# Performance work log

Hardware: AMD Instinct MI355X
Metric: run time of the kernel (lower is better)

The kernel has to match this reference:

```python
import jax, jax.numpy as jnp
import numpy as np

V = 8192
E = 262144
IN_DIM = 128
OUT_DIM = 128
NEG_SLOPE = 0.2


def setup_inputs() -> dict:
    key = jax.random.key(0)
    k1, k2, k3, k4 = jax.random.split(key, 4)
    h = jax.random.normal(k1, (V, IN_DIM), dtype=jnp.float32)
    edge_index = jax.random.randint(k2, (2, E), 0, V, dtype=jnp.int64)
    # nn.Linear weights: W (out_dim, in_dim), att (1, 2*out_dim), both bias-free
    W = jax.random.normal(k3, (OUT_DIM, IN_DIM), dtype=jnp.float32) / np.sqrt(IN_DIM)
    att_w = jax.random.normal(k4, (1, 2 * OUT_DIM), dtype=jnp.float32) / np.sqrt(2 * OUT_DIM)
    return {"h": h, "edge_index": edge_index, "W": W, "att_w": att_w}


def reference(h, edge_index, W, att_w):
    # h: (V, in_dim) -> (V, out_dim)
    hw = h @ W.T
    src, dst = edge_index[0], edge_index[1]
    # edge features: concat of endpoint embeddings -> (E, 2*out_dim)
    e = jnp.concatenate([hw[src], hw[dst]], axis=-1)
    # attention logits per edge, LeakyReLU(0.2)
    a = jax.nn.leaky_relu(jnp.squeeze(e @ att_w.T, -1), negative_slope=NEG_SLOPE)
    v = hw.shape[0]
    # faithful to original: dense V x V matrix, zeros on non-edges,
    # softmax over ALL columns (non-edges included as score 0)
    alpha = jnp.zeros((v, v), dtype=hw.dtype).at[src, dst].set(a)
    alpha = jax.nn.softmax(alpha, axis=-1)
    # dropout is identity in eval mode (deterministic reference)
    return alpha @ hw
```

## Files before the change

kernel.cpp:

```cpp
#include <hip/hip_runtime.h>
#include <hip/hip_bf16.h>
#include <math.h>


#define V 8192
#define E 262144
#define D 128
#define NEG_SLOPE 0.2f
#define CAP 96

#define FMA4(acc, hv, wv) { acc.x += (hv)*(wv).x; acc.y += (hv)*(wv).y; \
                            acc.z += (hv)*(wv).z; acc.w += (hv)*(wv).w; }

__device__ __forceinline__ unsigned short f2bf(float f) {
    unsigned u = __float_as_uint(f);
    return (unsigned short)((u + 0x7fffu + ((u >> 16) & 1u)) >> 16);
}
__device__ __forceinline__ float bf2f_low(int p) {
    return __uint_as_float(((unsigned)p) << 16);
}

__global__ __launch_bounds__(256) void k_hw(const float* __restrict__ h,
                                            const float* __restrict__ W,
                                            const float* __restrict__ att,
                                            unsigned short* __restrict__ hwb,
                                            float* __restrict__ s1,
                                            float* __restrict__ s2,
                                            float* __restrict__ Pb,
                                            int* __restrict__ cnt) {
    __shared__ float Wt[D * 132];
    __shared__ float hs[16][D];
    __shared__ float atts[2 * D];
    int t = threadIdx.x, b = blockIdx.x;
    int g0 = b * 256 + t;
    if (g0 < V) cnt[g0] = 0;
    atts[t] = att[t];
    for (int f4 = t; f4 < (D * D) / 4; f4 += 256) {
        int o = f4 >> 5, k = (f4 * 4) & 127;
        float4 wv = *(const float4*)&W[o * D + k];
        Wt[(k + 0) * 132 + o] = wv.x;
        Wt[(k + 1) * 132 + o] = wv.y;
        Wt[(k + 2) * 132 + o] = wv.z;
        Wt[(k + 3) * 132 + o] = wv.w;
    }
    int r0 = b * 16;
    {
        int row = t >> 5, col = (t * 4) & 127;
        *(float4*)&hs[row][col]     = *(const float4*)&h[(r0 + row) * D + col];
        *(float4*)&hs[row + 8][col] = *(const float4*)&h[(r0 + row + 8) * D + col];
    }
    __syncthreads();

    int c4 = (t & 31) * 4;
    int rq = t >> 5;
    float4 acc0 = make_float4(0.f, 0.f, 0.f, 0.f);
    float4 acc1 = make_float4(0.f, 0.f, 0.f, 0.f);
    #pragma unroll 2
    for (int kq = 0; kq < D; kq += 4) {
        float4 ha = *(const float4*)&hs[rq][kq];
        float4 hb = *(const float4*)&hs[rq + 8][kq];
        float4 w0 = *(const float4*)&Wt[(kq + 0) * 132 + c4];
        float4 w1 = *(const float4*)&Wt[(kq + 1) * 132 + c4];
        float4 w2 = *(const float4*)&Wt[(kq + 2) * 132 + c4];
        float4 w3 = *(const float4*)&Wt[(kq + 3) * 132 + c4];
        FMA4(acc0, ha.x, w0); FMA4(acc0, ha.y, w1);
        FMA4(acc0, ha.z, w2); FMA4(acc0, ha.w, w3);
        FMA4(acc1, hb.x, w0); FMA4(acc1, hb.y, w1);
        FMA4(acc1, hb.z, w2); FMA4(acc1, hb.w, w3);
    }
    int rowa = r0 + rq, rowb = r0 + rq + 8;
    ushort4 pa = make_ushort4(f2bf(acc0.x), f2bf(acc0.y), f2bf(acc0.z), f2bf(acc0.w));
    ushort4 pb = make_ushort4(f2bf(acc1.x), f2bf(acc1.y), f2bf(acc1.z), f2bf(acc1.w));
    *(ushort4*)&hwb[rowa * D + c4] = pa;
    *(ushort4*)&hwb[rowb * D + c4] = pb;

    float p1a = acc0.x * atts[c4] + acc0.y * atts[c4 + 1] + acc0.z * atts[c4 + 2] + acc0.w * atts[c4 + 3];
    float p2a = acc0.x * atts[D + c4] + acc0.y * atts[D + c4 + 1] + acc0.z * atts[D + c4 + 2] + acc0.w * atts[D + c4 + 3];
    float p1b = acc1.x * atts[c4] + acc1.y * atts[c4 + 1] + acc1.z * atts[c4 + 2] + acc1.w * atts[c4 + 3];
    float p2b = acc1.x * atts[D + c4] + acc1.y * atts[D + c4 + 1] + acc1.z * atts[D + c4 + 2] + acc1.w * atts[D + c4 + 3];
    #pragma unroll
    for (int m = 16; m; m >>= 1) {
        p1a += __shfl_xor(p1a, m); p2a += __shfl_xor(p2a, m);
        p1b += __shfl_xor(p1b, m); p2b += __shfl_xor(p2b, m);
    }
    if ((t & 31) == 0) {
        s1[rowa] = p1a; s2[rowa] = p2a;
        s1[rowb] = p1b; s2[rowb] = p2b;
    }

    __syncthreads();
    float* scr = &hs[0][0];
    scr[rq * D + c4 + 0] = acc0.x + acc1.x;
    scr[rq * D + c4 + 1] = acc0.y + acc1.y;
    scr[rq * D + c4 + 2] = acc0.z + acc1.z;
    scr[rq * D + c4 + 3] = acc0.w + acc1.w;
    __syncthreads();
    if (t < D) {
        float s = 0.f;
        #pragma unroll
        for (int r = 0; r < 8; ++r) s += scr[r * D + t];
        Pb[b * D + t] = s;
    }
}

__global__ __launch_bounds__(256) void k_scatter(const int* __restrict__ ei,
                                                 const float* __restrict__ s1,
                                                 const float* __restrict__ s2,
                                                 int* __restrict__ cnt,
                                                 int* __restrict__ bucket,
                                                 const float* __restrict__ Pb,
                                                 float* __restrict__ S) {
    int b = blockIdx.x, t = threadIdx.x;
    if (b < 256) {
        int g = b * 256 + t;
        int4 sv = *(const int4*)&ei[4 * g];
        int4 dv = *(const int4*)&ei[E + 4 * g];
        const int* sp = &sv.x;
        const int* dp = &dv.x;
        #pragma unroll
        for (int j = 0; j < 4; ++j) {
            int src = sp[j], dst = dp[j];
            float a = s1[src] + s2[dst];
            a = a > 0.f ? a : NEG_SLOPE * a;
            float w = expf(a) - 1.f;
            int pos = atomicAdd(&cnt[src], 1);
            if (pos < CAP)
                bucket[src * CAP + pos] = (dst << 16) | (int)f2bf(w);
        }
    } else {
        __shared__ float red[256];
        int c = t & 127, half = t >> 7;
        float s = 0.f;
        #pragma unroll 4
        for (int r = half; r < 512; r += 2)
            s += Pb[r * D + c];
        red[t] = s;
        __syncthreads();
        if (t < D) S[t] = red[t] + red[D + t];
    }
}

__global__ __launch_bounds__(256) void k_row(const int* __restrict__ bucket,
                                             const int* __restrict__ cnt,
                                             const unsigned short* __restrict__ hwb,
                                             const float* __restrict__ S,
                                             float* __restrict__ out) {
    int t = threadIdx.x;
    int wv = t >> 6, lane = t & 63;
    int row = blockIdx.x * 4 + wv;
    int deg = cnt[row];
    if (deg > CAP) deg = CAP;
    const int* bk = bucket + row * CAP;
    int e0 = bk[lane];
    int e1 = (lane < CAP - 64) ? bk[64 + lane] : 0;
    int p0 = (lane < deg)      ? e0 : (int)0xFFFF0000;
    int p1 = (64 + lane < deg) ? e1 : (int)0xFFFF0000;
    int d0 = p0 >> 16;
    int d1 = p1 >> 16;
    int n0 = deg < 64 ? deg : 64;
    float2 acc = make_float2(0.f, 0.f);
    float dex = 0.f;
    for (int j = 0; j < n0; ++j) {
        int pj = __shfl(p0, j);
        int dj = pj >> 16;
        float wj = bf2f_low(pj);
        unsigned long long m = __ballot(d0 == dj);
        if (m & ((1ull << j) - 1ull)) wj = 0.f;
        unsigned hv = *(const unsigned*)&hwb[dj * D + lane * 2];
        acc.x += wj * __uint_as_float(hv << 16);
        acc.y += wj * __uint_as_float(hv & 0xFFFF0000u);
        dex += wj;
    }
    for (int j = 64; j < deg; ++j) {
        int pj = __shfl(p1, j - 64);
        int dj = pj >> 16;
        float wj = bf2f_low(pj);
        unsigned long long m0 = __ballot(d0 == dj);
        unsigned long long m1 = __ballot(d1 == dj) & ((1ull << (j - 64)) - 1ull);
        if (m0 | m1) wj = 0.f;
        unsigned hv = *(const unsigned*)&hwb[dj * D + lane * 2];
        acc.x += wj * __uint_as_float(hv << 16);
        acc.y += wj * __uint_as_float(hv & 0xFFFF0000u);
        dex += wj;
    }
    float inv = 1.f / ((float)V + dex);
    float2 s = *(const float2*)&S[lane * 2];
    float2 o;
    o.x = (s.x + acc.x) * inv;
    o.y = (s.y + acc.y) * inv;
    *(float2*)&out[row * D + lane * 2] = o;
}

extern "C" void kernel_launch(void* const* d_in, const int* in_sizes, int n_in,
                              void* d_out, int out_size, void* d_ws, size_t ws_size,
                              hipStream_t stream) {
    const float* h   = (const float*)d_in[0];
    const int*   ei  = (const int*)d_in[1];
    const float* W   = (const float*)d_in[2];
    const float* att = (const float*)d_in[3];
    float* out = (float*)d_out;

    char* ws = (char*)d_ws;
    unsigned short* hwb = (unsigned short*)(ws);
    float* s1  = (float*)(ws + 2097152);
    float* s2  = (float*)(ws + 2129920);
    float* S   = (float*)(ws + 2162688);
    int*   cnt = (int*)(ws + 2163200);
    int*   bucket = (int*)(ws + 2195968);
    float* Pb  = (float*)(ws + 5341696);

    k_hw     <<<512,  256, 0, stream>>>(h, W, att, hwb, s1, s2, Pb, cnt);
    k_scatter<<<257,  256, 0, stream>>>(ei, s1, s2, cnt, bucket, Pb, S);
    k_row    <<<2048, 256, 0, stream>>>(bucket, cnt, hwb, S, out);
}
```

Baseline: 118.2 us.

## Rebalance hw tiling, one-edge-per-thread scatter, unroll row gather via LDS

The projection kernel now computes 32 rows per block with half the blocks, reading h directly from global memory, which halves the redundant W transpose work per row. The scatter kernel processes one edge per thread across four times as many blocks to spread the atomics out. The row kernel stages each row's bucket in shared memory and unrolls the neighbour gather by four so several hw loads are in flight at once. The trade-off is higher register pressure and uncoalesced global reads of h in the GEMM.

Result: faster. 106.0 us (-10.3%).

```diff
diff --git a/kernel.cpp b/kernel.cpp
--- a/kernel.cpp
+++ b/kernel.cpp
@@ -29,71 +29,78 @@
                                             float* __restrict__ Pb,
                                             int* __restrict__ cnt) {
     __shared__ float Wt[D * 132];
-    __shared__ float hs[16][D];
     __shared__ float atts[2 * D];
+    __shared__ float scr[8 * D];
     int t = threadIdx.x, b = blockIdx.x;
-    int g0 = b * 256 + t;
-    if (g0 < V) cnt[g0] = 0;
+    if (b < 32) cnt[b * 256 + t] = 0;
     atts[t] = att[t];
     for (int f4 = t; f4 < (D * D) / 4; f4 += 256) {
-        int o = f4 >> 5, k = (f4 * 4) & 127;
+        int o = f4 >> 5, k = (f4 & 31) * 4;
         float4 wv = *(const float4*)&W[o * D + k];
         Wt[(k + 0) * 132 + o] = wv.x;
         Wt[(k + 1) * 132 + o] = wv.y;
         Wt[(k + 2) * 132 + o] = wv.z;
         Wt[(k + 3) * 132 + o] = wv.w;
     }
-    int r0 = b * 16;
-    {
-        int row = t >> 5, col = (t * 4) & 127;
-        *(float4*)&hs[row][col]     = *(const float4*)&h[(r0 + row) * D + col];
-        *(float4*)&hs[row + 8][col] = *(const float4*)&h[(r0 + row + 8) * D + col];
-    }
     __syncthreads();
 
     int c4 = (t & 31) * 4;
     int rq = t >> 5;
-    float4 acc0 = make_float4(0.f, 0.f, 0.f, 0.f);
-    float4 acc1 = make_float4(0.f, 0.f, 0.f, 0.f);
-    #pragma unroll 2
+    int r0 = b * 32;
+    float4 a0 = make_float4(0.f,0.f,0.f,0.f), a1 = a0, a2 = a0, a3 = a0;
+    const float* h0p = &h[(r0 + rq     ) * D];
+    const float* h1p = &h[(r0 + rq +  8) * D];
+    const float* h2p = &h[(r0 + rq + 16) * D];
+    const float* h3p = &h[(r0 + rq + 24) * D];
+    #pragma unroll 4
     for (int kq = 0; kq < D; kq += 4) {
-        float4 ha = *(const float4*)&hs[rq][kq];
-        float4 hb = *(const float4*)&hs[rq + 8][kq];
         float4 w0 = *(const float4*)&Wt[(kq + 0) * 132 + c4];
         float4 w1 = *(const float4*)&Wt[(kq + 1) * 132 + c4];
         float4 w2 = *(const float4*)&Wt[(kq + 2) * 132 + c4];
         float4 w3 = *(const float4*)&Wt[(kq + 3) * 132 + c4];
-        FMA4(acc0, ha.x, w0); FMA4(acc0, ha.y, w1);
-        FMA4(acc0, ha.z, w2); FMA4(acc0, ha.w, w3);
-        FMA4(acc1, hb.x, w0); FMA4(acc1, hb.y, w1);
-        FMA4(acc1, hb.z, w2); FMA4(acc1, hb.w, w3);
-    }
-    int rowa = r0 + rq, rowb = r0 + rq + 8;
-    ushort4 pa = make_ushort4(f2bf(acc0.x), f2bf(acc0.y), f2bf(acc0.z), f2bf(acc0.w));
-    ushort4 pb = make_ushort4(f2bf(acc1.x), f2bf(acc1.y), f2bf(acc1.z), f2bf(acc1.w));
-    *(ushort4*)&hwb[rowa * D + c4] = pa;
-    *(ushort4*)&hwb[rowb * D + c4] = pb;
-
-    float p1a = acc0.x * atts[c4] + acc0.y * atts[c4 + 1] + acc0.z * atts[c4 + 2] + acc0.w * atts[c4 + 3];
-    float p2a = acc0.x * atts[D + c4] + acc0.y * atts[D + c4 + 1] + acc0.z * atts[D + c4 + 2] + acc0.w * atts[D + c4 + 3];
-    float p1b = acc1.x * atts[c4] + acc1.y * atts[c4 + 1] + acc1.z * atts[c4 + 2] + acc1.w * atts[c4 + 3];
-    float p2b = acc1.x * atts[D + c4] + acc1.y * atts[D + c4 + 1] + acc1.z * atts[D + c4 + 2] + acc1.w * atts[D + c4 + 3];
+        float4 hv;
+        hv = *(const float4*)&h0p[kq];
+        FMA4(a0, hv.x, w0); FMA4(a0, hv.y, w1); FMA4(a0, hv.z, w2); FMA4(a0, hv.w, w3);
+        hv = *(const float4*)&h1p[kq];
+        FMA4(a1, hv.x, w0); FMA4(a1, hv.y, w1); FMA4(a1, hv.z, w2); FMA4(a1, hv.w, w3);
+        hv = *(const float4*)&h2p[kq];
+        FMA4(a2, hv.x, w0); FMA4(a2, hv.y, w1); FMA4(a2, hv.z, w2); FMA4(a2, hv.w, w3);
+        hv = *(const float4*)&h3p[kq];
+        FMA4(a3, hv.x, w0); FMA4(a3, hv.y, w1); FMA4(a3, hv.z, w2); FMA4(a3, hv.w, w3);
+    }
+    *(ushort4*)&hwb[(r0 + rq     ) * D + c4] = make_ushort4(f2bf(a0.x), f2bf(a0.y), f2bf(a0.z), f2bf(a0.w));
+    *(ushort4*)&hwb[(r0 + rq +  8) * D + c4] = make_ushort4(f2bf(a1.x), f2bf(a1.y), f2bf(a1.z), f2bf(a1.w));
+    *(ushort4*)&hwb[(r0 + rq + 16) * D + c4] = make_ushort4(f2bf(a2.x), f2bf(a2.y), f2bf(a2.z), f2bf(a2.w));
+    *(ushort4*)&hwb[(r0 + rq + 24) * D + c4] = make_ushort4(f2bf(a3.x), f2bf(a3.y), f2bf(a3.z), f2bf(a3.w));
+
+    float q1[4], q2[4];
+    float4* accs[4] = {&a0, &a1, &a2, &a3};
+    #pragma unroll
+    for (int r = 0; r < 4; ++r) {
+        float4 v = *accs[r];
+        q1[r] = v.x * atts[c4] + v.y * atts[c4 + 1] + v.z * atts[c4 + 2] + v.w * atts[c4 + 3];
+        q2[r] = v.x * atts[D + c4] + v.y * atts[D + c4 + 1] + v.z * atts[D + c4 + 2] + v.w * atts[D + c4 + 3];
+    }
     #pragma unroll
     for (int m = 16; m; m >>= 1) {
-        p1a += __shfl_xor(p1a, m); p2a += __shfl_xor(p2a, m);
-        p1b += __shfl_xor(p1b, m); p2b += __shfl_xor(p2b, m);
+        #pragma unroll
+        for (int r = 0; r < 4; ++r) {
+            q1[r] += __shfl_xor(q1[r], m);
+            q2[r] += __shfl_xor(q2[r], m);
+        }
     }
     if ((t & 31) == 0) {
-        s1[rowa] = p1a; s2[rowa] = p2a;
-        s1[rowb] = p1b; s2[rowb] = p2b;
-    }
-
-    __syncthreads();
-    float* scr = &hs[0][0];
-    scr[rq * D + c4 + 0] = acc0.x + acc1.x;
-    scr[rq * D + c4 + 1] = acc0.y + acc1.y;
-    scr[rq * D + c4 + 2] = acc0.z + acc1.z;
-    scr[rq * D + c4 + 3] = acc0.w + acc1.w;
+        #pragma unroll
+        for (int r = 0; r < 4; ++r) {
+            s1[r0 + rq + r * 8] = q1[r];
+            s2[r0 + rq + r * 8] = q2[r];
+        }
+    }
+
+    scr[rq * D + c4 + 0] = a0.x + a1.x + a2.x + a3.x;
+    scr[rq * D + c4 + 1] = a0.y + a1.y + a2.y + a3.y;
+    scr[rq * D + c4 + 2] = a0.z + a1.z + a2.z + a3.z;
+    scr[rq * D + c4 + 3] = a0.w + a1.w + a2.w + a3.w;
     __syncthreads();
     if (t < D) {
         float s = 0.f;
@@ -111,28 +118,22 @@
                                                  const float* __restrict__ Pb,
                                                  float* __restrict__ S) {
     int b = blockIdx.x, t = threadIdx.x;
-    if (b < 256) {
+    if (b < 1024) {
         int g = b * 256 + t;
-        int4 sv = *(const int4*)&ei[4 * g];
-        int4 dv = *(const int4*)&ei[E + 4 * g];
-        const int* sp = &sv.x;
-        const int* dp = &dv.x;
-        #pragma unroll
-        for (int j = 0; j < 4; ++j) {
-            int src = sp[j], dst = dp[j];
-            float a = s1[src] + s2[dst];
-            a = a > 0.f ? a : NEG_SLOPE * a;
-            float w = expf(a) - 1.f;
-            int pos = atomicAdd(&cnt[src], 1);
-            if (pos < CAP)
-                bucket[src * CAP + pos] = (dst << 16) | (int)f2bf(w);
-        }
+        int src = ei[g];
+        int dst = ei[E + g];
+        float a = s1[src] + s2[dst];
+        a = a > 0.f ? a : NEG_SLOPE * a;
+        float w = expf(a) - 1.f;
+        int pos = atomicAdd(&cnt[src], 1);
+        if (pos < CAP)
+            bucket[src * CAP + pos] = (dst << 16) | (int)f2bf(w);
     } else {
         __shared__ float red[256];
         int c = t & 127, half = t >> 7;
         float s = 0.f;
         #pragma unroll 4
-        for (int r = half; r < 512; r += 2)
+        for (int r = half; r < 256; r += 2)
             s += Pb[r * D + c];
         red[t] = s;
         __syncthreads();
@@ -145,6 +146,7 @@
                                              const unsigned short* __restrict__ hwb,
                                              const float* __restrict__ S,
                                              float* __restrict__ out) {
+    __shared__ int lb[4][CAP];
     int t = threadIdx.x;
     int wv = t >> 6, lane = t & 63;
     int row = blockIdx.x * 4 + wv;
@@ -155,40 +157,69 @@
     int e1 = (lane < CAP - 64) ? bk[64 + lane] : 0;
     int p0 = (lane < deg)      ? e0 : (int)0xFFFF0000;
     int p1 = (64 + lane < deg) ? e1 : (int)0xFFFF0000;
+    lb[wv][lane] = p0;
+    if (lane < CAP - 64) lb[wv][64 + lane] = p1;
     int d0 = p0 >> 16;
     int d1 = p1 >> 16;
     int n0 = deg < 64 ? deg : 64;
-    float2 acc = make_float2(0.f, 0.f);
-    float dex = 0.f;
-    for (int j = 0; j < n0; ++j) {
-        int pj = __shfl(p0, j);
+    float accx = 0.f, accy = 0.f, dex = 0.f;
+    const int* myb = lb[wv];
+    int col2 = lane * 2;
+    int j = 0;
+    for (; j + 4 <= n0; j += 4) {
+        int4 pq = *(const int4*)&myb[j];
+        int dj0 = pq.x >> 16, dj1 = pq.y >> 16, dj2 = pq.z >> 16, dj3 = pq.w >> 16;
+        unsigned hv0 = *(const unsigned*)&hwb[dj0 * D + col2];
+        unsigned hv1 = *(const unsigned*)&hwb[dj1 * D + col2];
+        unsigned hv2 = *(const unsigned*)&hwb[dj2 * D + col2];
+        unsigned hv3 = *(const unsigned*)&hwb[dj3 * D + col2];
+        unsigned long long m0 = __ballot(d0 == dj0);
+        unsigned long long m1 = __ballot(d0 == dj1);
+        unsigned long long m2 = __ballot(d0 == dj2);
+        unsigned long long m3 = __ballot(d0 == dj3);
+        float w0 = (m0 & ((1ull << (j + 0)) - 1ull)) ? 0.f : bf2f_low(pq.x);
+        float w1 = (m1 & ((1ull << (j + 1)) - 1ull)) ? 0.f : bf2f_low(pq.y);
+        float w2 = (m2 & ((1ull << (j + 2)) - 1ull)) ? 0.f : bf2f_low(pq.z);
+        float w3 = (m3 & ((1ull << (j + 3)) - 1ull)) ? 0.f : bf2f_low(pq.w);
+        accx += w0 * __uint_as_float(hv0 << 16);
+        accy += w0 * __uint_as_float(hv0 & 0xFFFF0000u);
+        accx += w1 * __uint_as_float(hv1 << 16);
+        accy += w1 * __uint_as_float(hv1 & 0xFFFF0000u);
+        accx += w2 * __uint_as_float(hv2 << 16);
+        accy += w2 * __uint_as_float(hv2 & 0xFFFF0000u);
+        accx += w3 * __uint_as_float(hv3 << 16);
+        accy += w3 * __uint_as_float(hv3 & 0xFFFF0000u);
+        dex += w0 + w1 + w2 + w3;
+    }
+    for (; j < n0; ++j) {
+        int pj = myb[j];
         int dj = pj >> 16;
         float wj = bf2f_low(pj);
         unsigned long long m = __ballot(d0 == dj);
         if (m & ((1ull << j) - 1ull)) wj = 0.f;
-        unsigned hv = *(const unsigned*)&hwb[dj * D + lane * 2];
-        acc.x += wj * __uint_as_float(hv << 16);
-        acc.y += wj * __uint_as_float(hv & 0xFFFF0000u);
+        unsigned hv = *(const unsigned*)&hwb[dj * D + col2];
+        accx += wj * __uint_as_float(hv << 16);
+        accy += wj * __uint_as_float(hv & 0xFFFF0000u);
         dex += wj;
     }
-    for (int j = 64; j < deg; ++j) {
-        int pj = __shfl(p1, j - 64);
+    for (j = 64; j < deg; ++j) {
+        int pj = myb[j];
         int dj = pj >> 16;
         float wj = bf2f_low(pj);
         unsigned long long m0 = __ballot(d0 == dj);
         unsigned long long m1 = __ballot(d1 == dj) & ((1ull << (j - 64)) - 1ull);
         if (m0 | m1) wj = 0.f;
-        unsigned hv = *(const unsigned*)&hwb[dj * D + lane * 2];
-        acc.x += wj * __uint_as_float(hv << 16);
-        acc.y += wj * __uint_as_float(hv & 0xFFFF0000u);
+        unsigned hv = *(const unsigned*)&hwb[dj * D + col2];
+        accx += wj * __uint_as_float(hv << 16);
+        accy += wj * __uint_as_float(hv & 0xFFFF0000u);
         dex += wj;
     }
     float inv = 1.f / ((float)V + dex);
-    float2 s = *(const float2*)&S[lane * 2];
+    float2 s = *(const float2*)&S[col2];
     float2 o;
-    o.x = (s.x + acc.x) * inv;
-    o.y = (s.y + acc.y) * inv;
-    *(float2*)&out[row * D + lane * 2] = o;
+    o.x = (s.x + accx) * inv;
+    o.y = (s.y + accy) * inv;
+    *(float2*)&out[row * D + col2] = o;
 }
 
 extern "C" void kernel_launch(void* const* d_in, const int* in_sizes, int n_in,
@@ -209,7 +240,7 @@
     int*   bucket = (int*)(ws + 2195968);
     float* Pb  = (float*)(ws + 5341696);
 
-    k_hw     <<<512,  256, 0, stream>>>(h, W, att, hwb, s1, s2, Pb, cnt);
-    k_scatter<<<257,  256, 0, stream>>>(ei, s1, s2, cnt, bucket, Pb, S);
+    k_hw     <<<256,  256, 0, stream>>>(h, W, att, hwb, s1, s2, Pb, cnt);
+    k_scatter<<<1025, 256, 0, stream>>>(ei, s1, s2, cnt, bucket, Pb, S);
     k_row    <<<2048, 256, 0, stream>>>(bucket, cnt, hwb, S, out);
 }
```
